# Kernel optimization log

Measured on AMD Instinct MI355X. Metric: run time of the kernel, lower is better.

## Reference

```python
import jax, jax.numpy as jnp
import numpy as np

DIM = 1024
N_EXPERTS = 8
TOP_K = 2
HIDDEN = 2730  # int(2 * (dim*4) / 3)


def setup_inputs() -> dict:
    key = jax.random.key(0)
    k1, k2, k3, k4 = jax.random.split(key, 4)
    x = jax.random.normal(k1, (4, 2048, DIM), dtype=jnp.float32)
    Wr = jax.random.normal(k2, (DIM, N_EXPERTS), dtype=jnp.float32) * 0.02
    W12 = jax.random.normal(k3, (N_EXPERTS, DIM, 2 * HIDDEN), dtype=jnp.float32) * 0.02
    W3 = jax.random.normal(k4, (N_EXPERTS, HIDDEN, DIM), dtype=jnp.float32) * 0.02
    return {"x": x, "Wr": Wr, "W12": W12, "W3": W3}


def reference(x, Wr, W12, W3):
    # x: [B, S, D]; eval-mode MoE forward (no load-balancing adjustment).
    B, S, D = x.shape
    xf = x.reshape(-1, D)                       # [T, D]
    logits = xf @ Wr                            # [T, E]
    top_vals, top_idx = jax.lax.top_k(logits, TOP_K)  # [T, K]
    top_w = jax.nn.softmax(top_vals, axis=-1)   # [T, K]
    out = jnp.zeros_like(xf)
    for e in range(N_EXPERTS):
        # combined gate weight for tokens routed to expert e (0 if not routed)
        gate = jnp.sum(jnp.where(top_idx == e, top_w, 0.0), axis=-1)  # [T]
        h12 = xf @ W12[e]                       # [T, 2H]
        h1, h2 = jnp.split(h12, 2, axis=-1)
        eo = (jax.nn.silu(h1) * h2) @ W3[e]     # [T, D]
        out = out + gate[:, None] * eo
    return out.reshape(B, S, D)
```

## Files before the change

kernel.cpp:

```cpp
#include <hip/hip_runtime.h>


typedef __bf16 bf16x8 __attribute__((ext_vector_type(8)));
typedef float f32x4 __attribute__((ext_vector_type(4)));
typedef unsigned short us8 __attribute__((ext_vector_type(8)));

#define T_TOK 8192
#define DIMD 1024
#define NEXP 8
#define HID 2730
#define HPAD 2752
#define H2PAD 5504
#define NPAIR 16384

#define WS_CTRL  ((size_t)0)
#define WS_TOPI  ((size_t)256)
#define WS_TOPW  (WS_TOPI + 65536)
#define WS_POS   (WS_TOPW + 65536)
#define WS_PTOK  (WS_POS + 65536)
#define WS_XB    (WS_PTOK + 65536)
#define WS_W12T  (WS_XB + (size_t)16777216)
#define WS_W3T   (WS_W12T + (size_t)90177536)
#define WS_HBUF  (WS_W3T + (size_t)45088768)
#define WS_POUT  (WS_HBUF + (size_t)90177536)

#define GLOAD16(g, l) __builtin_amdgcn_global_load_lds( \
    (const __attribute__((address_space(1))) void*)(g), \
    (__attribute__((address_space(3))) void*)(l), 16, 0, 0)

__device__ __forceinline__ unsigned short f2bf(float f) {
    unsigned int u = __float_as_uint(f);
    u += 0x7fffu + ((u >> 16) & 1u);
    return (unsigned short)(u >> 16);
}

__global__ void k_cvt_all(const float* __restrict__ w12, const float* __restrict__ w3,
                          unsigned short* __restrict__ w12t, unsigned short* __restrict__ w3t) {
    __shared__ float tile[64][129];
    int t = threadIdx.x;
    int lane16 = t & 15, rowgrp = t >> 4;
    int bid = blockIdx.x;
    if (bid < 5504) {
        int b = bid;
        int kt = b & 7; b >>= 3;
        int jt = b % 43; b /= 43;
        int half = b & 1, e = b >> 1;
        int jh0 = jt * 64, k0 = kt * 128;
        int j = jh0 + lane16 * 4;
        const float* srcb = w12 + (size_t)(e * 1024 + k0) * 5460 + half * HID + j;
        if (jh0 + 64 <= HID) {
#pragma unroll
            for (int p = 0; p < 8; ++p) {
                int kk = p * 16 + rowgrp;
                f32x4 v = *(const f32x4*)(srcb + (size_t)kk * 5460);
                tile[lane16 * 4][kk] = v[0];
                tile[lane16 * 4 + 1][kk] = v[1];
                tile[lane16 * 4 + 2][kk] = v[2];
                tile[lane16 * 4 + 3][kk] = v[3];
            }
        } else {
#pragma unroll
            for (int p = 0; p < 8; ++p) {
                int kk = p * 16 + rowgrp;
#pragma unroll
                for (int i = 0; i < 4; ++i) {
                    float v = 0.f;
                    if (j + i < HID) v = srcb[(size_t)kk * 5460 + i];
                    tile[lane16 * 4 + i][kk] = v;
                }
            }
        }
        __syncthreads();
        unsigned short* dstb = w12t + ((size_t)e * H2PAD + half * HPAD + jh0) * 1024 + k0 + lane16 * 8;
#pragma unroll
        for (int q = 0; q < 4; ++q) {
            int jl = q * 16 + rowgrp;
            us8 v;
#pragma unroll
            for (int b8 = 0; b8 < 8; ++b8) v[b8] = f2bf(tile[jl][lane16 * 8 + b8]);
            *(us8*)(dstb + (size_t)jl * 1024) = v;
        }
    } else {
        int b2 = bid - 5504;
        int kt = b2 % 22; b2 /= 22;
        int dt = b2 & 15, e = b2 >> 4;
        int d0 = dt * 64, k0 = kt * 128;
        int d = d0 + lane16 * 4;
        const float* srcb = w3 + (size_t)(e * HID) * 1024 + d;
#pragma unroll
        for (int p = 0; p < 8; ++p) {
            int kk = k0 + p * 16 + rowgrp;
            f32x4 v = {0.f, 0.f, 0.f, 0.f};
            if (kk < HID) v = *(const f32x4*)(srcb + (size_t)kk * 1024);
            tile[lane16 * 4][p * 16 + rowgrp] = v[0];
            tile[lane16 * 4 + 1][p * 16 + rowgrp] = v[1];
            tile[lane16 * 4 + 2][p * 16 + rowgrp] = v[2];
            tile[lane16 * 4 + 3][p * 16 + rowgrp] = v[3];
        }
        __syncthreads();
        if (k0 + lane16 * 8 + 8 <= HPAD) {
            unsigned short* dstb = w3t + ((size_t)e * 1024 + d0) * HPAD + k0 + lane16 * 8;
#pragma unroll
            for (int q = 0; q < 4; ++q) {
                int dl = q * 16 + rowgrp;
                us8 v;
#pragma unroll
                for (int b8 = 0; b8 < 8; ++b8) v[b8] = f2bf(tile[dl][lane16 * 8 + b8]);
                *(us8*)(dstb + (size_t)dl * HPAD) = v;
            }
        }
    }
}

__global__ void k_router(const float4* __restrict__ x4, const float* __restrict__ wr,
                         ushort4* __restrict__ xb4,
                         int* __restrict__ topi, float* __restrict__ topw) {
    int wid = threadIdx.x >> 6, lane = threadIdx.x & 63;
    int t = blockIdx.x * 4 + wid;
    const float4* xr = x4 + (size_t)t * 256;
    double acc[NEXP];
#pragma unroll
    for (int e = 0; e < NEXP; ++e) acc[e] = 0.0;
#pragma unroll
    for (int it = 0; it < 4; ++it) {
        int d4 = it * 64 + lane;
        float4 v = xr[d4];
        ushort4 r;
        r.x = f2bf(v.x); r.y = f2bf(v.y); r.z = f2bf(v.z); r.w = f2bf(v.w);
        xb4[(size_t)t * 256 + d4] = r;
        const float* w = wr + (size_t)d4 * 4 * NEXP;
#pragma unroll
        for (int e = 0; e < NEXP; ++e) {
            acc[e] += (double)v.x * (double)w[e]
                    + (double)v.y * (double)w[NEXP + e]
                    + (double)v.z * (double)w[2 * NEXP + e]
                    + (double)v.w * (double)w[3 * NEXP + e];
        }
    }
#pragma unroll
    for (int e = 0; e < NEXP; ++e) {
        for (int off = 32; off > 0; off >>= 1) acc[e] += __shfl_down(acc[e], off);
    }
    if (lane == 0) {
        double b0 = -1e300, b1 = -1e300; int i0 = 0, i1 = 0;
#pragma unroll
        for (int e = 0; e < NEXP; ++e) {
            double v = acc[e];
            if (v > b0) { b1 = b0; i1 = i0; b0 = v; i0 = e; }
            else if (v > b1) { b1 = v; i1 = e; }
        }
        float e1 = expf((float)(b1 - b0));
        float w0 = 1.0f / (1.0f + e1);
        float w1 = e1 / (1.0f + e1);
        topi[2 * t] = i0; topi[2 * t + 1] = i1;
        topw[2 * t] = w0; topw[2 * t + 1] = w1;
    }
}

__global__ __launch_bounds__(1024) void k_pack(const int* __restrict__ topi,
                                               int* __restrict__ ctrl,
                                               int* __restrict__ ptok,
                                               int* __restrict__ pos) {
    __shared__ int scnt[NEXP][1024];
    __shared__ int offs[NEXP];
    int tid = threadIdx.x;
    int lc[NEXP];
#pragma unroll
    for (int e = 0; e < NEXP; ++e) lc[e] = 0;
    int t0 = tid * 8;
#pragma unroll
    for (int i = 0; i < 8; ++i) {
        int t = t0 + i;
        lc[topi[2 * t]]++;
        lc[topi[2 * t + 1]]++;
    }
#pragma unroll
    for (int e = 0; e < NEXP; ++e) scnt[e][tid] = lc[e];
    __syncthreads();
    for (int off = 1; off < 1024; off <<= 1) {
        int v[NEXP];
#pragma unroll
        for (int e = 0; e < NEXP; ++e) v[e] = (tid >= off) ? scnt[e][tid - off] : 0;
        __syncthreads();
#pragma unroll
        for (int e = 0; e < NEXP; ++e) scnt[e][tid] += v[e];
        __syncthreads();
    }
    if (tid == 0) {
        int s = 0;
#pragma unroll
        for (int e = 0; e < NEXP; ++e) {
            int c = scnt[e][1023];
            ctrl[e] = c;
            ctrl[16 + e] = s;
            offs[e] = s;
            s += c;
        }
        ctrl[16 + NEXP] = s;
    }
    __syncthreads();
    int r[NEXP];
#pragma unroll
    for (int e = 0; e < NEXP; ++e) r[e] = offs[e] + scnt[e][tid] - lc[e];
#pragma unroll
    for (int i = 0; i < 8; ++i) {
        int t = t0 + i;
#pragma unroll
        for (int k = 0; k < 2; ++k) {
            int e = topi[2 * t + k];
            int p = r[e]++;
            ptok[p] = t;
            pos[2 * t + k] = p;
        }
    }
}

#define G1_STAGE(S) do { \
    GLOAD16(aSrc0, ALp + (S) * 8192 + wid * 512); aSrc0 += 64; \
    GLOAD16(aSrc1, ALp + (S) * 8192 + 4096 + wid * 512); aSrc1 += 64; \
    GLOAD16(bSrc, BLp + (S) * 4096 + wid * 512); bSrc += 64; \
} while (0)

#define G1_STEP(CUR, STG, WAITSTR, DOSTAGE) do { \
    asm volatile("s_waitcnt " WAITSTR ::: "memory"); \
    __builtin_amdgcn_s_barrier(); \
    if (DOSTAGE) G1_STAGE(STG); \
    const unsigned short* Ab = ALp + (CUR) * 8192 + cSwz; \
    const unsigned short* Bb = BLp + (CUR) * 4096 + cSwz; \
    bf16x8 af[4], bfr[2][2]; \
    _Pragma("unroll") \
    for (int m = 0; m < 4; ++m) af[m] = *(const bf16x8*)(Ab + aoff[m]); \
    _Pragma("unroll") \
    for (int h = 0; h < 2; ++h) \
        _Pragma("unroll") \
        for (int n = 0; n < 2; ++n) bfr[h][n] = *(const bf16x8*)(Bb + boff[h][n]); \
    __builtin_amdgcn_s_setprio(1); \
    _Pragma("unroll") \
    for (int h = 0; h < 2; ++h) \
        _Pragma("unroll") \
        for (int m = 0; m < 4; ++m) \
            _Pragma("unroll") \
            for (int n = 0; n < 2; ++n) \
                acc[m][h][n] = __builtin_amdgcn_mfma_f32_16x16x32_bf16( \
                    af[m], bfr[h][n], acc[m][h][n], 0, 0, 0); \
    __builtin_amdgcn_s_setprio(0); \
} while (0)

__global__ __launch_bounds__(512, 4) void k_gemm1(
    const unsigned short* __restrict__ xb,
    const unsigned short* __restrict__ w12t,
    const int* __restrict__ ctrl,
    const int* __restrict__ ptok,
    unsigned short* __restrict__ hbuf) {
    int e = blockIdx.z;
    int n_e = ctrl[e];
    int r0 = blockIdx.y * 256;
    if (r0 >= n_e) return;
    int p0 = ctrl[16 + e] + r0;
    int j0 = blockIdx.x * 64;

    __shared__ unsigned short AL[3][256][32];
    __shared__ unsigned short BL[3][128][32];

    int tid = threadIdx.x, lane = tid & 63, wid = tid >> 6;
    int wm = wid >> 1, wn = wid & 1;
    int lr = lane & 15, lk = lane >> 4;

    unsigned short* ALp = &AL[0][0][0];
    unsigned short* BLp = &BL[0][0][0];

    int swzB = (((tid & 3) ^ ((tid >> 3) & 3)) << 4);
    const char* aSrc0;
    const char* aSrc1;
    {
        int row0 = (tid >> 2);
        int row1 = 128 + (tid >> 2);
        int tok0 = (r0 + row0 < n_e) ? ptok[p0 + row0] : ptok[p0];
        int tok1 = (r0 + row1 < n_e) ? ptok[p0 + row1] : ptok[p0];
        aSrc0 = (const char*)(xb + (size_t)tok0 * 1024) + swzB;
        aSrc1 = (const char*)(xb + (size_t)tok1 * 1024) + swzB;
    }
    const char* bSrc;
    {
        int r = tid >> 2;
        int half = r >> 6, jj = r & 63;
        bSrc = (const char*)(w12t + ((size_t)e * H2PAD + half * HPAD + j0 + jj) * 1024) + swzB;
    }

    f32x4 acc[4][2][2];
#pragma unroll
    for (int m = 0; m < 4; ++m)
#pragma unroll
        for (int h = 0; h < 2; ++h)
#pragma unroll
            for (int n = 0; n < 2; ++n) acc[m][h][n] = (f32x4){0.f, 0.f, 0.f, 0.f};

    int cSwz = ((lk ^ ((lr >> 1) & 3)) << 3);
    int aoff[4], boff[2][2];
#pragma unroll
    for (int m = 0; m < 4; ++m) aoff[m] = (wm * 64 + m * 16 + lr) * 32;
#pragma unroll
    for (int h = 0; h < 2; ++h)
#pragma unroll
        for (int n = 0; n < 2; ++n) boff[h][n] = (h * 64 + wn * 32 + n * 16 + lr) * 32;

    G1_STAGE(0);
    G1_STAGE(1);

#pragma unroll 1
    for (int t3 = 0; t3 < 10; ++t3) {
        G1_STEP(0, 2, "vmcnt(3)", true);
        G1_STEP(1, 0, "vmcnt(3)", true);
        G1_STEP(2, 1, "vmcnt(3)", true);
    }
    G1_STEP(0, 2, "vmcnt(3)", false);
    G1_STEP(1, 0, "vmcnt(0)", false);

#pragma unroll
    for (int m = 0; m < 4; ++m)
#pragma unroll
        for (int n = 0; n < 2; ++n)
#pragma unroll
            for (int q = 0; q < 4; ++q) {
                int rl = wm * 64 + m * 16 + lk * 4 + q;
                if (r0 + rl < n_e) {
                    float v1 = acc[m][0][n][q];
                    float v2 = acc[m][1][n][q];
                    float hv = v1 * (1.0f / (1.0f + __expf(-v1))) * v2;
                    hbuf[(size_t)(p0 + rl) * HPAD + (j0 + wn * 32 + n * 16 + lr)] = f2bf(hv);
                }
            }
}

#define G2_STEP(CUR, STG, WAITSTR, DOSTAGE) do { \
    asm volatile("s_waitcnt " WAITSTR ::: "memory"); \
    __builtin_amdgcn_s_barrier(); \
    if (DOSTAGE) G1_STAGE(STG); \
    const unsigned short* Ab = ALp + (CUR) * 8192 + cSwz; \
    const unsigned short* Bb = BLp + (CUR) * 4096 + cSwz; \
    bf16x8 af[4], bfr[4]; \
    _Pragma("unroll") \
    for (int m = 0; m < 4; ++m) af[m] = *(const bf16x8*)(Ab + aoff[m]); \
    _Pragma("unroll") \
    for (int n = 0; n < 4; ++n) bfr[n] = *(const bf16x8*)(Bb + boff[n]); \
    __builtin_amdgcn_s_setprio(1); \
    _Pragma("unroll") \
    for (int m = 0; m < 4; ++m) \
        _Pragma("unroll") \
        for (int n = 0; n < 4; ++n) \
            acc[m][n] = __builtin_amdgcn_mfma_f32_16x16x32_bf16( \
                af[m], bfr[n], acc[m][n], 0, 0, 0); \
    __builtin_amdgcn_s_setprio(0); \
} while (0)

__global__ __launch_bounds__(512, 4) void k_gemm2(
    const unsigned short* __restrict__ hbuf,
    const unsigned short* __restrict__ w3t,
    const int* __restrict__ ctrl,
    float* __restrict__ pout) {
    int e = blockIdx.z;
    int n_e = ctrl[e];
    int r0 = blockIdx.y * 256;
    if (r0 >= n_e) return;
    int p0 = ctrl[16 + e] + r0;
    int d0 = blockIdx.x * 128;

    __shared__ unsigned short AL[3][256][32];
    __shared__ unsigned short BL[3][128][32];

    int tid = threadIdx.x, lane = tid & 63, wid = tid >> 6;
    int wm = wid >> 1, wn = wid & 1;
    int lr = lane & 15, lk = lane >> 4;

    unsigned short* ALp = &AL[0][0][0];
    unsigned short* BLp = &BL[0][0][0];

    int swzB = (((tid & 3) ^ ((tid >> 3) & 3)) << 4);
    const char* aSrc0;
    const char* aSrc1;
    {
        int row0 = (tid >> 2);
        int row1 = 128 + (tid >> 2);
        int arr0 = (r0 + row0 < n_e) ? row0 : 0;
        int arr1 = (r0 + row1 < n_e) ? row1 : 0;
        aSrc0 = (const char*)(hbuf + (size_t)(p0 + arr0) * HPAD) + swzB;
        aSrc1 = (const char*)(hbuf + (size_t)(p0 + arr1) * HPAD) + swzB;
    }
    const char* bSrc = (const char*)(w3t + ((size_t)e * 1024 + d0 + (tid >> 2)) * HPAD) + swzB;

    f32x4 acc[4][4];
#pragma unroll
    for (int m = 0; m < 4; ++m)
#pragma unroll
        for (int n = 0; n < 4; ++n) acc[m][n] = (f32x4){0.f, 0.f, 0.f, 0.f};

    int cSwz = ((lk ^ ((lr >> 1) & 3)) << 3);
    int aoff[4], boff[4];
#pragma unroll
    for (int m = 0; m < 4; ++m) aoff[m] = (wm * 64 + m * 16 + lr) * 32;
#pragma unroll
    for (int n = 0; n < 4; ++n) boff[n] = (wn * 64 + n * 16 + lr) * 32;

    G1_STAGE(0);
    G1_STAGE(1);

#pragma unroll 1
    for (int t3 = 0; t3 < 28; ++t3) {
        G2_STEP(0, 2, "vmcnt(3)", true);
        G2_STEP(1, 0, "vmcnt(3)", true);
        G2_STEP(2, 1, "vmcnt(3)", true);
    }
    G2_STEP(0, 2, "vmcnt(3)", false);
    G2_STEP(1, 0, "vmcnt(0)", false);

#pragma unroll
    for (int m = 0; m < 4; ++m) {
        int rl0 = wm * 64 + m * 16 + lk * 4;
#pragma unroll
        for (int q = 0; q < 4; ++q) {
            int rl = rl0 + q;
            if (r0 + rl < n_e) {
                float* orow = pout + (size_t)(p0 + rl) * DIMD + d0;
#pragma unroll
                for (int n = 0; n < 4; ++n) {
                    orow[wn * 64 + n * 16 + lr] = acc[m][n][q];
                }
            }
        }
    }
}

__global__ void k_combine(const float4* __restrict__ pout, const int* __restrict__ pos,
                          const float* __restrict__ topw, float4* __restrict__ out) {
    int idx = blockIdx.x * 256 + threadIdx.x;
    int tok = idx >> 8, c = idx & 255;
    int p0 = pos[2 * tok], p1 = pos[2 * tok + 1];
    float w0 = topw[2 * tok], w1 = topw[2 * tok + 1];
    float4 a = pout[(size_t)p0 * 256 + c];
    float4 b = pout[(size_t)p1 * 256 + c];
    float4 r;
    r.x = w0 * a.x + w1 * b.x;
    r.y = w0 * a.y + w1 * b.y;
    r.z = w0 * a.z + w1 * b.z;
    r.w = w0 * a.w + w1 * b.w;
    out[idx] = r;
}

extern "C" void kernel_launch(void* const* d_in, const int* in_sizes, int n_in,
                              void* d_out, int out_size, void* d_ws, size_t ws_size,
                              hipStream_t stream) {
    const float* x   = (const float*)d_in[0];
    const float* wr  = (const float*)d_in[1];
    const float* w12 = (const float*)d_in[2];
    const float* w3  = (const float*)d_in[3];
    float* out = (float*)d_out;

    char* ws = (char*)d_ws;
    int*            ctrl = (int*)(ws + WS_CTRL);
    int*            topi = (int*)(ws + WS_TOPI);
    float*          topw = (float*)(ws + WS_TOPW);
    int*            pos  = (int*)(ws + WS_POS);
    int*            ptok = (int*)(ws + WS_PTOK);
    unsigned short* xb   = (unsigned short*)(ws + WS_XB);
    unsigned short* w12t = (unsigned short*)(ws + WS_W12T);
    unsigned short* w3t  = (unsigned short*)(ws + WS_W3T);
    unsigned short* hbuf = (unsigned short*)(ws + WS_HBUF);
    float*          pout = (float*)(ws + WS_POUT);

    (void)ws_size; (void)in_sizes; (void)n_in; (void)out_size;

    k_cvt_all<<<8320, 256, 0, stream>>>(w12, w3, w12t, w3t);
    k_router<<<2048, 256, 0, stream>>>((const float4*)x, wr, (ushort4*)xb, topi, topw);
    k_pack<<<1, 1024, 0, stream>>>(topi, ctrl, ptok, pos);
    k_gemm1<<<dim3(43, 32, 8), 512, 0, stream>>>(xb, w12t, ctrl, ptok, hbuf);
    k_gemm2<<<dim3(8, 32, 8), 512, 0, stream>>>(hbuf, w3t, ctrl, pout);
    k_combine<<<8192, 256, 0, stream>>>((const float4*)pout, pos, topw, (float4*)out);
}
```

Baseline: 542.1 us.

## Fold gate weight into GEMM1 and scatter GEMM2 output with atomics

The routing gate weight is now applied in the GEMM1 epilogue, written per packed row by the pack kernel. GEMM2 scatter-adds its results straight into the zeroed output with float atomics. This removes the separate combine kernel and the fp32 pout round trip through memory. In exchange it adds a memset and per-element global atomics, and the summation order becomes nondeterministic.

```diff
diff --git a/kernel.cpp b/kernel.cpp
--- a/kernel.cpp
+++ b/kernel.cpp
@@ -16,13 +16,12 @@
 #define WS_CTRL  ((size_t)0)
 #define WS_TOPI  ((size_t)256)
 #define WS_TOPW  (WS_TOPI + 65536)
-#define WS_POS   (WS_TOPW + 65536)
-#define WS_PTOK  (WS_POS + 65536)
+#define WS_PW    (WS_TOPW + 65536)
+#define WS_PTOK  (WS_PW + 65536)
 #define WS_XB    (WS_PTOK + 65536)
 #define WS_W12T  (WS_XB + (size_t)16777216)
 #define WS_W3T   (WS_W12T + (size_t)90177536)
 #define WS_HBUF  (WS_W3T + (size_t)45088768)
-#define WS_POUT  (WS_HBUF + (size_t)90177536)
 
 #define GLOAD16(g, l) __builtin_amdgcn_global_load_lds( \
     (const __attribute__((address_space(1))) void*)(g), \
@@ -158,9 +157,10 @@
 }
 
 __global__ __launch_bounds__(1024) void k_pack(const int* __restrict__ topi,
+                                               const float* __restrict__ topw,
                                                int* __restrict__ ctrl,
                                                int* __restrict__ ptok,
-                                               int* __restrict__ pos) {
+                                               float* __restrict__ pw) {
     __shared__ int scnt[NEXP][1024];
     __shared__ int offs[NEXP];
     int tid = threadIdx.x;
@@ -210,7 +210,7 @@
             int e = topi[2 * t + k];
             int p = r[e]++;
             ptok[p] = t;
-            pos[2 * t + k] = p;
+            pw[p] = topw[2 * t + k];
         }
     }
 }
@@ -251,6 +251,7 @@
     const unsigned short* __restrict__ w12t,
     const int* __restrict__ ctrl,
     const int* __restrict__ ptok,
+    const float* __restrict__ pw,
     unsigned short* __restrict__ hbuf) {
     int e = blockIdx.z;
     int n_e = ctrl[e];
@@ -319,17 +320,19 @@
 #pragma unroll
     for (int m = 0; m < 4; ++m)
 #pragma unroll
-        for (int n = 0; n < 2; ++n)
-#pragma unroll
-            for (int q = 0; q < 4; ++q) {
-                int rl = wm * 64 + m * 16 + lk * 4 + q;
-                if (r0 + rl < n_e) {
+        for (int q = 0; q < 4; ++q) {
+            int rl = wm * 64 + m * 16 + lk * 4 + q;
+            if (r0 + rl < n_e) {
+                float w = pw[p0 + rl];
+#pragma unroll
+                for (int n = 0; n < 2; ++n) {
                     float v1 = acc[m][0][n][q];
                     float v2 = acc[m][1][n][q];
-                    float hv = v1 * (1.0f / (1.0f + __expf(-v1))) * v2;
+                    float hv = w * (v1 * (1.0f / (1.0f + __expf(-v1))) * v2);
                     hbuf[(size_t)(p0 + rl) * HPAD + (j0 + wn * 32 + n * 16 + lr)] = f2bf(hv);
                 }
             }
+        }
 }
 
 #define G2_STEP(CUR, STG, WAITSTR, DOSTAGE) do { \
@@ -357,7 +360,8 @@
     const unsigned short* __restrict__ hbuf,
     const unsigned short* __restrict__ w3t,
     const int* __restrict__ ctrl,
-    float* __restrict__ pout) {
+    const int* __restrict__ ptok,
+    float* __restrict__ out) {
     int e = blockIdx.z;
     int n_e = ctrl[e];
     int r0 = blockIdx.y * 256;
@@ -420,30 +424,15 @@
         for (int q = 0; q < 4; ++q) {
             int rl = rl0 + q;
             if (r0 + rl < n_e) {
-                float* orow = pout + (size_t)(p0 + rl) * DIMD + d0;
+                int tok = ptok[p0 + rl];
+                float* orow = out + (size_t)tok * DIMD + d0;
 #pragma unroll
                 for (int n = 0; n < 4; ++n) {
-                    orow[wn * 64 + n * 16 + lr] = acc[m][n][q];
+                    atomicAdd(orow + (wn * 64 + n * 16 + lr), acc[m][n][q]);
                 }
             }
         }
     }
-}
-
-__global__ void k_combine(const float4* __restrict__ pout, const int* __restrict__ pos,
-                          const float* __restrict__ topw, float4* __restrict__ out) {
-    int idx = blockIdx.x * 256 + threadIdx.x;
-    int tok = idx >> 8, c = idx & 255;
-    int p0 = pos[2 * tok], p1 = pos[2 * tok + 1];
-    float w0 = topw[2 * tok], w1 = topw[2 * tok + 1];
-    float4 a = pout[(size_t)p0 * 256 + c];
-    float4 b = pout[(size_t)p1 * 256 + c];
-    float4 r;
-    r.x = w0 * a.x + w1 * b.x;
-    r.y = w0 * a.y + w1 * b.y;
-    r.z = w0 * a.z + w1 * b.z;
-    r.w = w0 * a.w + w1 * b.w;
-    out[idx] = r;
 }
 
 extern "C" void kernel_launch(void* const* d_in, const int* in_sizes, int n_in,
@@ -459,20 +448,19 @@
     int*            ctrl = (int*)(ws + WS_CTRL);
     int*            topi = (int*)(ws + WS_TOPI);
     float*          topw = (float*)(ws + WS_TOPW);
-    int*            pos  = (int*)(ws + WS_POS);
+    float*          pw   = (float*)(ws + WS_PW);
     int*            ptok = (int*)(ws + WS_PTOK);
     unsigned short* xb   = (unsigned short*)(ws + WS_XB);
     unsigned short* w12t = (unsigned short*)(ws + WS_W12T);
     unsigned short* w3t  = (unsigned short*)(ws + WS_W3T);
     unsigned short* hbuf = (unsigned short*)(ws + WS_HBUF);
-    float*          pout = (float*)(ws + WS_POUT);
 
     (void)ws_size; (void)in_sizes; (void)n_in; (void)out_size;
 
+    (void)hipMemsetAsync(out, 0, (size_t)T_TOK * DIMD * sizeof(float), stream);
     k_cvt_all<<<8320, 256, 0, stream>>>(w12, w3, w12t, w3t);
     k_router<<<2048, 256, 0, stream>>>((const float4*)x, wr, (ushort4*)xb, topi, topw);
-    k_pack<<<1, 1024, 0, stream>>>(topi, ctrl, ptok, pos);
-    k_gemm1<<<dim3(43, 32, 8), 512, 0, stream>>>(xb, w12t, ctrl, ptok, hbuf);
-    k_gemm2<<<dim3(8, 32, 8), 512, 0, stream>>>(hbuf, w3t, ctrl, pout);
-    k_combine<<<8192, 256, 0, stream>>>((const float4*)pout, pos, topw, (float4*)out);
-}
+    k_pack<<<1, 1024, 0, stream>>>(topi, topw, ctrl, ptok, pw);
+    k_gemm1<<<dim3(43, 32, 8), 512, 0, stream>>>(xb, w12t, ctrl, ptok, pw, hbuf);
+    k_gemm2<<<dim3(8, 32, 8), 512, 0, stream>>>(hbuf, w3t, ctrl, ptok, out);
+}
```

Measured after the change: 557.3 us. 1.03x slower.
